# Kernel optimization log

Measured on AMD Instinct MI355X. Metric: run time of the kernel, lower is better.

## Reference

```python
import jax, jax.numpy as jnp
import numpy as np

H = 384  # LSTMCell features per layer
REVS = (True, False, True, False, True)  # reverse flags per layer (keep_order=True restores order)


def _lstm_layer(x, Wi, Wh, b, rev):
    # x: [B, T, D]; Wi: [D, 4H]; Wh: [H, 4H]; b: [4H]
    # flax nn.RNN(reverse=True, keep_order=True) == flip input, scan, flip output.
    if rev:
        x = x[:, ::-1]
    xT = jnp.swapaxes(x, 0, 1)            # [T, B, D]
    xproj = xT @ Wi + b                    # precompute input projection: [T, B, 4H]
    B = x.shape[0]
    c0 = jnp.zeros((B, H), x.dtype)
    h0 = jnp.zeros((B, H), x.dtype)

    def step(carry, xp):
        c, h = carry
        z = xp + h @ Wh                    # [B, 4H]
        i, f, g, o = jnp.split(z, 4, axis=-1)
        c = jax.nn.sigmoid(f) * c + jax.nn.sigmoid(i) * jnp.tanh(g)
        h = jax.nn.sigmoid(o) * jnp.tanh(c)
        return (c, h), h

    _, hs = jax.lax.scan(step, (c0, h0), xproj)  # hs: [T, B, H]
    out = jnp.swapaxes(hs, 0, 1)                 # [B, T, H]
    if rev:
        out = out[:, ::-1]
    return out


def setup_inputs() -> dict:
    key = jax.random.key(0)
    k_x, k_wi, k_wh = jax.random.split(key, 3)
    B, T, D = 64, 1024, 384
    x = jax.random.normal(k_x, (B, T, D), dtype=jnp.float32)
    # flax LSTMCell: input dense (no bias) + recurrent dense (with bias); bias init zeros.
    Wi = jax.random.normal(k_wi, (5, D, 4 * H), dtype=jnp.float32) * 0.05
    Wh = jax.random.normal(k_wh, (5, H, 4 * H), dtype=jnp.float32) * 0.05
    b = jnp.zeros((5, 4 * H), dtype=jnp.float32)
    return {"x": x, "Wi": Wi, "Wh": Wh, "b": b}


def reference(x, Wi, Wh, b):
    for l, rev in enumerate(REVS):
        x = _lstm_layer(x, Wi[l], Wh[l], b[l], rev)
    return x
```

## Files before the change

kernel.cpp:

```cpp
#include <hip/hip_runtime.h>
#include <cstdint>
#include <cstddef>


#define T_SEQ   1024
#define DD      384
#define HH      384
#define FH      1536
#define NBATCH  64
#define BG      8
#define CC      24
#define JHW     16
#define RTHREADS 512
#define SMEM_BYTES 129664

typedef unsigned long long u64;

__device__ __forceinline__ float sigmoidf_(float x) {
  return 1.0f / (1.0f + __expf(-x));
}
__device__ __forceinline__ float tanhf_(float x) {
  float ax = fabsf(x);
  float e  = __expf(-2.0f * ax);
  float r  = (1.0f - e) / (1.0f + e);
  return (x >= 0.0f) ? r : -r;
}

__global__ __launch_bounds__(256) void gemm_xproj(
    const float* __restrict__ xin, const float* __restrict__ Wi,
    const float* __restrict__ bias, float* __restrict__ xproj,
    int t0, int rev)
{
  __shared__ float As[8][132];
  __shared__ float Bs[8][132];

  const int tid = threadIdx.x;
  const int tx = tid & 15, ty = tid >> 4;

  const int nyb = gridDim.x / 12;
  int bx, by;
  if ((nyb & 7) == 0) {
    const int xcd   = blockIdx.x & 7;
    const int s     = blockIdx.x >> 3;
    const int chunk = nyb >> 3;
    by = xcd * chunk + s / 12;
    bx = s % 12;
  } else {
    bx = blockIdx.x % 12;
    by = blockIdx.x / 12;
  }
  const int m0 = by * 128;
  const int j0 = bx * 128;

  const int r    = tid >> 1;
  const int part = tid & 1;
  const int m    = m0 + r;
  const int b    = m & 63;
  const int trel = m >> 6;
  const int t    = t0 + trel;
  const int tsrc = rev ? (T_SEQ - 1 - t) : t;
  const float* arow = xin + ((size_t)b * T_SEQ + tsrc) * DD + part * 4;

  const int kr = tid >> 5;
  const int jc = (tid & 31) << 2;
  const float* brow = Wi + (size_t)kr * FH + j0 + jc;

  float acc[8][8];
#pragma unroll
  for (int i = 0; i < 8; ++i)
#pragma unroll
    for (int j = 0; j < 8; ++j) acc[i][j] = 0.0f;

  float4 av = *(const float4*)(arow);
  float4 bv = *(const float4*)(brow);

  for (int kt = 0; kt < 48; ++kt) {
    __syncthreads();
    As[part * 4 + 0][r] = av.x;
    As[part * 4 + 1][r] = av.y;
    As[part * 4 + 2][r] = av.z;
    As[part * 4 + 3][r] = av.w;
    *(float4*)&Bs[kr][jc] = bv;
    __syncthreads();
    if (kt < 47) {
      av = *(const float4*)(arow + (kt + 1) * 8);
      bv = *(const float4*)(brow + (size_t)(kt + 1) * 8 * FH);
    }
#pragma unroll
    for (int k = 0; k < 8; ++k) {
      float a[8], bb[8];
      *(float4*)&a[0]  = *(const float4*)&As[k][ty * 8];
      *(float4*)&a[4]  = *(const float4*)&As[k][ty * 8 + 4];
      *(float4*)&bb[0] = *(const float4*)&Bs[k][tx * 8];
      *(float4*)&bb[4] = *(const float4*)&Bs[k][tx * 8 + 4];
#pragma unroll
      for (int i = 0; i < 8; ++i)
#pragma unroll
        for (int j = 0; j < 8; ++j)
          acc[i][j] = fmaf(a[i], bb[j], acc[i][j]);
    }
  }

  float bvals[8];
#pragma unroll
  for (int j = 0; j < 8; ++j) bvals[j] = bias[j0 + tx * 8 + j];

#pragma unroll
  for (int i = 0; i < 8; ++i) {
    const int mm = m0 + ty * 8 + i;
    float* orow = xproj + (size_t)mm * FH + j0 + tx * 8;
    float4 o0, o1;
    o0.x = acc[i][0] + bvals[0]; o0.y = acc[i][1] + bvals[1];
    o0.z = acc[i][2] + bvals[2]; o0.w = acc[i][3] + bvals[3];
    o1.x = acc[i][4] + bvals[4]; o1.y = acc[i][5] + bvals[5];
    o1.z = acc[i][6] + bvals[6]; o1.w = acc[i][7] + bvals[7];
    *(float4*)(orow)     = o0;
    *(float4*)(orow + 4) = o1;
  }
}

__global__ __launch_bounds__(RTHREADS) void lstm_recur(
    const float* __restrict__ xp, const float* __restrict__ Wh,
    float* __restrict__ xout, u64* __restrict__ h_ex,
    float* __restrict__ c_state,
    int t0, int Tc, int rev, int layer)
{
  extern __shared__ char smem[];
  float (*WhL)[64]  = (float (*)[64])(smem);
  float (*hL)[388]  = (float (*)[388])(smem + 98304);
  float* zred       = (float*)(smem + 110720);
  float* cL         = (float*)(smem + 129152);

  const int wg   = blockIdx.x;
  const int bg   = wg & 7;
  const int cc   = wg >> 3;
  const int tid  = threadIdx.x;
  const int wave = tid >> 6;
  const int lane = tid & 63;
  const unsigned base = (unsigned)(layer * 1025);

  for (int idx = tid; idx < 384 * 64; idx += RTHREADS) {
    int k = idx >> 6;
    int c = idx & 63;
    int col = ((c >> 4) * HH) + cc * JHW + (c & 15);
    WhL[k][c] = Wh[(size_t)k * FH + col];
  }

  const int rb    = tid >> 4;
  const int rjj   = tid & 15;
  const int bglob = bg * BG + rb;
  const int hb    = cc * JHW + rjj;

  if (tid < 128) {
    cL[tid] = (t0 == 0) ? 0.0f : c_state[(size_t)bglob * HH + hb];
    if (t0 == 0) {
      u64 pack = ((u64)base << 32);
      __hip_atomic_store(&h_ex[(size_t)(NBATCH * HH) + (size_t)bglob * HH + hb],
                         pack, __ATOMIC_RELAXED, __HIP_MEMORY_SCOPE_AGENT);
    }
  }
  __syncthreads();

  const int k0 = wave * 48;

  for (int tr = 0; tr < Tc; ++tr) {
    const int t = t0 + tr;

    float xpr0 = 0.f, xpr1 = 0.f, xpr2 = 0.f, xpr3 = 0.f;
    if (tid < 128) {
      const float* xr = xp + ((size_t)tr * NBATCH + bglob) * FH + cc * JHW + rjj;
      xpr0 = xr[0];
      xpr1 = xr[384];
      xpr2 = xr[768];
      xpr3 = xr[1152];
    }

    {
      const unsigned tagT = base + (unsigned)t;
      const u64* hsrc = h_ex + (size_t)((t + 1) & 1) * (NBATCH * HH)
                             + (size_t)bg * BG * HH;
      u64 v[6];
#pragma unroll
      for (int k = 0; k < 6; ++k)
        v[k] = __hip_atomic_load(&hsrc[tid + k * RTHREADS],
                                 __ATOMIC_RELAXED, __HIP_MEMORY_SCOPE_AGENT);
#pragma unroll
      for (int k = 0; k < 6; ++k) {
        while ((unsigned)(v[k] >> 32) != tagT) {
          v[k] = __hip_atomic_load(&hsrc[tid + k * RTHREADS],
                                   __ATOMIC_RELAXED, __HIP_MEMORY_SCOPE_AGENT);
        }
        const int e  = tid + k * RTHREADS;
        const int bb = e / HH;
        const int cl = e - bb * HH;
        hL[bb][cl] = __uint_as_float((unsigned)v[k]);
      }
    }
    __syncthreads();

    float acc[8] = {0, 0, 0, 0, 0, 0, 0, 0};
#pragma unroll 4
    for (int q = 0; q < 12; ++q) {
      const int k = k0 + q * 4;
      const float w0 = WhL[k][lane];
      const float w1 = WhL[k + 1][lane];
      const float w2 = WhL[k + 2][lane];
      const float w3 = WhL[k + 3][lane];
#pragma unroll
      for (int bb = 0; bb < 8; ++bb) {
        float4 h4 = *(const float4*)&hL[bb][k];
        acc[bb] = fmaf(w0, h4.x, acc[bb]);
        acc[bb] = fmaf(w1, h4.y, acc[bb]);
        acc[bb] = fmaf(w2, h4.z, acc[bb]);
        acc[bb] = fmaf(w3, h4.w, acc[bb]);
      }
    }
#pragma unroll
    for (int bb = 0; bb < 8; ++bb)
      zred[(bb * 64 + lane) * 9 + wave] = acc[bb];
    __syncthreads();

    if (tid < 128) {
      float zi = xpr0, zf = xpr1, zg = xpr2, zo = xpr3;
#pragma unroll
      for (int w = 0; w < 8; ++w) {
        zi += zred[(rb * 64 +  0 + rjj) * 9 + w];
        zf += zred[(rb * 64 + 16 + rjj) * 9 + w];
        zg += zred[(rb * 64 + 32 + rjj) * 9 + w];
        zo += zred[(rb * 64 + 48 + rjj) * 9 + w];
      }
      float c = cL[tid];
      c = sigmoidf_(zf) * c + sigmoidf_(zi) * tanhf_(zg);
      float h = sigmoidf_(zo) * tanhf_(c);
      cL[tid] = c;
      u64 pack = ((u64)(base + (unsigned)t + 1u) << 32)
               | (u64)__float_as_uint(h);
      __hip_atomic_store(&h_ex[(size_t)(t & 1) * (NBATCH * HH)
                               + (size_t)bglob * HH + hb],
                         pack, __ATOMIC_RELAXED, __HIP_MEMORY_SCOPE_AGENT);
      const int to = rev ? (T_SEQ - 1 - t) : t;
      xout[((size_t)bglob * T_SEQ + to) * HH + hb] = h;
    }
  }

  if (tid < 128) {
    c_state[(size_t)bglob * HH + hb] = cL[tid];
  }
}

extern "C" void kernel_launch(void* const* d_in, const int* in_sizes, int n_in,
                              void* d_out, int out_size, void* d_ws, size_t ws_size,
                              hipStream_t stream) {
  (void)in_sizes; (void)n_in; (void)out_size;

  const float* x  = (const float*)d_in[0];
  const float* Wi = (const float*)d_in[1];
  const float* Wh = (const float*)d_in[2];
  const float* bs = (const float*)d_in[3];
  float* out = (float*)d_out;

  char*  ws      = (char*)d_ws;
  float* c_state = (float*)ws;
  u64*   h_ex    = (u64*)(ws + 98304);
  float* xproj   = (float*)(ws + 98304 + 393216);
  const size_t fixed = 98304 + 393216;

  int Tc = 1024;
  while (Tc > 8 && fixed + (size_t)Tc * NBATCH * FH * 4 > ws_size) Tc >>= 1;

  (void)hipFuncSetAttribute((const void*)lstm_recur,
                            hipFuncAttributeMaxDynamicSharedMemorySize,
                            SMEM_BYTES);

  const int revs[5] = {1, 0, 1, 0, 1};
  for (int l = 0; l < 5; ++l) {
    const float* xin = (l == 0) ? x : out;
    for (int t0 = 0; t0 < T_SEQ; t0 += Tc) {
      const int nyb = (Tc * NBATCH) / 128;
      gemm_xproj<<<dim3(nyb * 12), 256, 0, stream>>>(
          xin, Wi + (size_t)l * DD * FH,
          bs + (size_t)l * FH, xproj, t0, revs[l]);
      lstm_recur<<<192, RTHREADS, SMEM_BYTES, stream>>>(
          xproj, Wh + (size_t)l * DD * FH, out, h_ex, c_state,
          t0, Tc, revs[l], l);
    }
  }
}
```

Before: 32.64 ms.

## Keep recurrent weights in registers and double-buffer the projection GEMM tiles

The recurrent kernel now holds each thread's 48 Wh weights in registers instead of reading them from LDS every step. This cuts LDS traffic and shrinks dynamic shared memory to about 31 KB, so the max-shared-memory attribute is no longer set. A barrier is added at the end of each timestep to guard reuse of hL and zred. The input-projection GEMM gets double-buffered LDS tiles with one barrier per k-step and a min-blocks launch bound. The cost is higher register pressure, which could cause spills.

```diff
diff --git a/kernel.cpp b/kernel.cpp
--- a/kernel.cpp
+++ b/kernel.cpp
@@ -12,7 +12,7 @@
 #define CC      24
 #define JHW     16
 #define RTHREADS 512
-#define SMEM_BYTES 129664
+#define RSMEM_BYTES 31360
 
 typedef unsigned long long u64;
 
@@ -26,13 +26,13 @@
   return (x >= 0.0f) ? r : -r;
 }
 
-__global__ __launch_bounds__(256) void gemm_xproj(
+__global__ __launch_bounds__(256, 3) void gemm_xproj(
     const float* __restrict__ xin, const float* __restrict__ Wi,
     const float* __restrict__ bias, float* __restrict__ xproj,
     int t0, int rev)
 {
-  __shared__ float As[8][132];
-  __shared__ float Bs[8][132];
+  __shared__ float As[2][8][132];
+  __shared__ float Bs[2][8][132];
 
   const int tid = threadIdx.x;
   const int tx = tid & 15, ty = tid >> 4;
@@ -71,33 +71,45 @@
 #pragma unroll
     for (int j = 0; j < 8; ++j) acc[i][j] = 0.0f;
 
-  float4 av = *(const float4*)(arow);
-  float4 bv = *(const float4*)(brow);
+  {
+    float4 av = *(const float4*)(arow);
+    float4 bv = *(const float4*)(brow);
+    As[0][part * 4 + 0][r] = av.x;
+    As[0][part * 4 + 1][r] = av.y;
+    As[0][part * 4 + 2][r] = av.z;
+    As[0][part * 4 + 3][r] = av.w;
+    *(float4*)&Bs[0][kr][jc] = bv;
+  }
+  __syncthreads();
 
   for (int kt = 0; kt < 48; ++kt) {
-    __syncthreads();
-    As[part * 4 + 0][r] = av.x;
-    As[part * 4 + 1][r] = av.y;
-    As[part * 4 + 2][r] = av.z;
-    As[part * 4 + 3][r] = av.w;
-    *(float4*)&Bs[kr][jc] = bv;
-    __syncthreads();
+    const int cur = kt & 1;
+    float4 av2, bv2;
     if (kt < 47) {
-      av = *(const float4*)(arow + (kt + 1) * 8);
-      bv = *(const float4*)(brow + (size_t)(kt + 1) * 8 * FH);
+      av2 = *(const float4*)(arow + (kt + 1) * 8);
+      bv2 = *(const float4*)(brow + (size_t)(kt + 1) * 8 * FH);
     }
 #pragma unroll
     for (int k = 0; k < 8; ++k) {
       float a[8], bb[8];
-      *(float4*)&a[0]  = *(const float4*)&As[k][ty * 8];
-      *(float4*)&a[4]  = *(const float4*)&As[k][ty * 8 + 4];
-      *(float4*)&bb[0] = *(const float4*)&Bs[k][tx * 8];
-      *(float4*)&bb[4] = *(const float4*)&Bs[k][tx * 8 + 4];
+      *(float4*)&a[0]  = *(const float4*)&As[cur][k][ty * 8];
+      *(float4*)&a[4]  = *(const float4*)&As[cur][k][ty * 8 + 4];
+      *(float4*)&bb[0] = *(const float4*)&Bs[cur][k][tx * 8];
+      *(float4*)&bb[4] = *(const float4*)&Bs[cur][k][tx * 8 + 4];
 #pragma unroll
       for (int i = 0; i < 8; ++i)
 #pragma unroll
         for (int j = 0; j < 8; ++j)
           acc[i][j] = fmaf(a[i], bb[j], acc[i][j]);
+    }
+    if (kt < 47) {
+      const int nxt = cur ^ 1;
+      As[nxt][part * 4 + 0][r] = av2.x;
+      As[nxt][part * 4 + 1][r] = av2.y;
+      As[nxt][part * 4 + 2][r] = av2.z;
+      As[nxt][part * 4 + 3][r] = av2.w;
+      *(float4*)&Bs[nxt][kr][jc] = bv2;
+      __syncthreads();
     }
   }
 
@@ -126,10 +138,9 @@
     int t0, int Tc, int rev, int layer)
 {
   extern __shared__ char smem[];
-  float (*WhL)[64]  = (float (*)[64])(smem);
-  float (*hL)[388]  = (float (*)[388])(smem + 98304);
-  float* zred       = (float*)(smem + 110720);
-  float* cL         = (float*)(smem + 129152);
+  float (*hL)[388] = (float (*)[388])(smem);
+  float* zred      = (float*)(smem + 12416);
+  float* cL        = (float*)(smem + 30848);
 
   const int wg   = blockIdx.x;
   const int bg   = wg & 7;
@@ -138,13 +149,13 @@
   const int wave = tid >> 6;
   const int lane = tid & 63;
   const unsigned base = (unsigned)(layer * 1025);
-
-  for (int idx = tid; idx < 384 * 64; idx += RTHREADS) {
-    int k = idx >> 6;
-    int c = idx & 63;
-    int col = ((c >> 4) * HH) + cc * JHW + (c & 15);
-    WhL[k][c] = Wh[(size_t)k * FH + col];
-  }
+  const int k0 = wave * 48;
+
+  const int colg = ((lane >> 4) * HH) + cc * JHW + (lane & 15);
+  float wreg[48];
+#pragma unroll
+  for (int q = 0; q < 48; ++q)
+    wreg[q] = Wh[(size_t)(k0 + q) * FH + colg];
 
   const int rb    = tid >> 4;
   const int rjj   = tid & 15;
@@ -160,8 +171,6 @@
     }
   }
   __syncthreads();
-
-  const int k0 = wave * 48;
 
   for (int tr = 0; tr < Tc; ++tr) {
     const int t = t0 + tr;
@@ -199,20 +208,16 @@
     __syncthreads();
 
     float acc[8] = {0, 0, 0, 0, 0, 0, 0, 0};
-#pragma unroll 4
-    for (int q = 0; q < 12; ++q) {
-      const int k = k0 + q * 4;
-      const float w0 = WhL[k][lane];
-      const float w1 = WhL[k + 1][lane];
-      const float w2 = WhL[k + 2][lane];
-      const float w3 = WhL[k + 3][lane];
+#pragma unroll
+    for (int q4 = 0; q4 < 12; ++q4) {
+      const int k = q4 * 4;
 #pragma unroll
       for (int bb = 0; bb < 8; ++bb) {
-        float4 h4 = *(const float4*)&hL[bb][k];
-        acc[bb] = fmaf(w0, h4.x, acc[bb]);
-        acc[bb] = fmaf(w1, h4.y, acc[bb]);
-        acc[bb] = fmaf(w2, h4.z, acc[bb]);
-        acc[bb] = fmaf(w3, h4.w, acc[bb]);
+        float4 h4 = *(const float4*)&hL[bb][k0 + k];
+        acc[bb] = fmaf(wreg[k],     h4.x, acc[bb]);
+        acc[bb] = fmaf(wreg[k + 1], h4.y, acc[bb]);
+        acc[bb] = fmaf(wreg[k + 2], h4.z, acc[bb]);
+        acc[bb] = fmaf(wreg[k + 3], h4.w, acc[bb]);
       }
     }
 #pragma unroll
@@ -241,6 +246,7 @@
       const int to = rev ? (T_SEQ - 1 - t) : t;
       xout[((size_t)bglob * T_SEQ + to) * HH + hb] = h;
     }
+    __syncthreads();
   }
 
   if (tid < 128) {
@@ -267,10 +273,6 @@
 
   int Tc = 1024;
   while (Tc > 8 && fixed + (size_t)Tc * NBATCH * FH * 4 > ws_size) Tc >>= 1;
-
-  (void)hipFuncSetAttribute((const void*)lstm_recur,
-                            hipFuncAttributeMaxDynamicSharedMemorySize,
-                            SMEM_BYTES);
 
   const int revs[5] = {1, 0, 1, 0, 1};
   for (int l = 0; l < 5; ++l) {
@@ -280,7 +282,7 @@
       gemm_xproj<<<dim3(nyb * 12), 256, 0, stream>>>(
           xin, Wi + (size_t)l * DD * FH,
           bs + (size_t)l * FH, xproj, t0, revs[l]);
-      lstm_recur<<<192, RTHREADS, SMEM_BYTES, stream>>>(
+      lstm_recur<<<192, RTHREADS, RSMEM_BYTES, stream>>>(
           xproj, Wh + (size_t)l * DD * FH, out, h_ex, c_state,
           t0, Tc, revs[l], l);
     }
```

After: 29.51 ms. 9.6% less time.
